# Kernel optimization log

Measured on AMD Instinct MI355X. Metric: run time of the kernel, lower is better.

## Reference

```python
import jax, jax.numpy as jnp
from jax import lax
import numpy as np

G = 18          # grid_dim
NB = 1.0        # num_bins
SIG = 0.6       # sigma
NA = 6          # num_atoms
B = 64          # structures in batch
APB = 512       # atoms per structure
N = B * APB
SIGP2 = 2.0 * (SIG * NB) ** 2  # 2*sigma_p^2


def setup_inputs() -> dict:
    key = jax.random.key(0)
    ks = list(jax.random.split(key, 24))
    # structured atom tensor: sorted batch idx, random atom type, uniform coords
    bidx = jnp.repeat(jnp.arange(B), APB).astype(jnp.float32)
    atype = jax.random.randint(ks[0], (N,), 0, NA).astype(jnp.float32)
    pos = jax.random.uniform(ks[1], (N, 3), minval=-8.5, maxval=8.5)
    x = jnp.concatenate([bidx[:, None], atype[:, None], pos], axis=1)

    def w(k, shape, fan_in):
        return jax.random.normal(k, shape, jnp.float32) * (1.0 / np.sqrt(fan_in))

    d = {"x": x, "batch_size": B}
    chans = [(6, 16), (16, 32), (32, 64)]
    for i, (ci, co) in enumerate(chans):
        d[f"conv_w{i}"] = w(ks[2 + i], (co, ci, 3, 3, 3), ci * 27)
        d[f"conv_b{i}"] = jnp.zeros((co,), jnp.float32)
        d[f"bn_g{i}"] = jnp.ones((co,), jnp.float32)
        d[f"bn_b{i}"] = jnp.zeros((co,), jnp.float32)
    d["mlp_w0"] = w(ks[10], (512, 512), 512); d["mlp_b0"] = jnp.zeros((512,), jnp.float32)
    d["bn1_g"] = jnp.ones((512,), jnp.float32); d["bn1_b"] = jnp.zeros((512,), jnp.float32)
    d["mlp_w1"] = w(ks[11], (256, 512), 512); d["mlp_b1"] = jnp.zeros((256,), jnp.float32)
    d["bn2_g"] = jnp.ones((256,), jnp.float32); d["bn2_b"] = jnp.zeros((256,), jnp.float32)
    d["mlp_w2"] = w(ks[12], (100, 256), 256); d["mlp_b2"] = jnp.zeros((100,), jnp.float32)
    d["head_w"] = w(ks[13], (20, 100), 100); d["head_b"] = jnp.zeros((20,), jnp.float32)
    return d


def _leaky(v):
    return jnp.where(v >= 0, v, 0.01 * v)  # LeakyReLU(0.01)


def _bn(v, g, b, axes):
    # train-mode batchnorm: batch stats, biased var, eps=1e-5; channel axis = 1
    m = v.mean(axes, keepdims=True)
    var = v.var(axes, keepdims=True)
    sh = [1] * v.ndim
    sh[1] = -1
    return (v - m) / jnp.sqrt(var + 1e-5) * g.reshape(sh) + b.reshape(sh)


def _blur(x, batch_size):
    # gaussian_blurring: per-atom normalized gaussian splat onto [B, NA, G, G, G]
    grid = jnp.linspace(-G / 2 * NB + NB / 2, G / 2 * NB - NB / 2, G)
    xx, yy, zz = jnp.meshgrid(grid, grid, grid, indexing='ij')
    coords = jnp.stack([xx.ravel(), yy.ravel(), zz.ravel()], axis=1)  # [V,3]
    pos = x[:, 2:5]                                                   # [N,3]
    # squared distances [N,V] via expansion (avoids [N,V,3] intermediate)
    d2 = ((pos ** 2).sum(1, keepdims=True)
          + (coords ** 2).sum(1)[None, :]
          - 2.0 * pos @ coords.T)
    dens = jnp.exp(-d2 / SIGP2)                         # [N,V]
    dens = dens / (dens.sum(1, keepdims=True) + 1e-6)   # normalize per atom over voxels
    seg = x[:, 0].astype(jnp.int32) * NA + x[:, 1].astype(jnp.int32)
    fields = jax.ops.segment_sum(dens, seg, num_segments=batch_size * NA)
    return fields.reshape(batch_size, NA, G, G, G)


def _forward(x, batch_size, conv_w0, conv_b0, bn_g0, bn_b0, conv_w1, conv_b1, bn_g1, bn_b1,
             conv_w2, conv_b2, bn_g2, bn_b2, mlp_w0, mlp_b0, bn1_g, bn1_b,
             mlp_w1, mlp_b1, bn2_g, bn2_b, mlp_w2, mlp_b2, head_w, head_b):
    h = _blur(x, batch_size)  # [B,6,18,18,18]
    for cw, cb, g, b in ((conv_w0, conv_b0, bn_g0, bn_b0),
                         (conv_w1, conv_b1, bn_g1, bn_b1),
                         (conv_w2, conv_b2, bn_g2, bn_b2)):
        h = lax.conv_general_dilated(h, cw, (1, 1, 1), 'SAME',
                                     dimension_numbers=('NCDHW', 'OIDHW', 'NCDHW'))
        h = h + cb[None, :, None, None, None]
        h = lax.reduce_window(h, -jnp.inf, lax.max, (1, 1, 2, 2, 2), (1, 1, 2, 2, 2), 'VALID')
        h = _leaky(_bn(h, g, b, (0, 2, 3, 4)))
    h = h.reshape(h.shape[0], -1)                                   # [B,512]
    h = _leaky(_bn(h @ mlp_w0.T + mlp_b0, bn1_g, bn1_b, (0,)))
    h = _leaky(_bn(h @ mlp_w1.T + mlp_b1, bn2_g, bn2_b, (0,)))
    h = h @ mlp_w2.T + mlp_b2                                       # [B,100]
    return _leaky(h) @ head_w.T + head_b                            # header -> [B,20]


def reference(x, batch_size, conv_w0, conv_b0, bn_g0, bn_b0, conv_w1, conv_b1, bn_g1, bn_b1,
              conv_w2, conv_b2, bn_g2, bn_b2, mlp_w0, mlp_b0, bn1_g, bn1_b,
              mlp_w1, mlp_b1, bn2_g, bn2_b, mlp_w2, mlp_b2, head_w, head_b):
    return _forward(x, batch_size, conv_w0, conv_b0, bn_g0, bn_b0, conv_w1, conv_b1,
                    bn_g1, bn_b1, conv_w2, conv_b2, bn_g2, bn_b2, mlp_w0, mlp_b0,
                    bn1_g, bn1_b, mlp_w1, mlp_b1, bn2_g, bn2_b, mlp_w2, mlp_b2,
                    head_w, head_b)
```

## Files before the change

### kernel.cpp

```cpp
#include <hip/hip_runtime.h>
#include <math.h>

#define BATCH 64
#define APB 512
#define NA 6
#define NG 5832

__device__ __forceinline__ float leaky(float v){ return v >= 0.f ? v : 0.01f*v; }

__global__ __launch_bounds__(64) void atom_sort(const float* __restrict__ x,
                                                int* __restrict__ dst,
                                                int* __restrict__ seg_start,
                                                int* __restrict__ seg_count)
{
  int batch = blockIdx.x;
  int lane  = threadIdx.x;
  int tyc[8];
  int cnt[NA];
  #pragma unroll
  for (int t = 0; t < NA; t++) cnt[t] = 0;
  #pragma unroll
  for (int c = 0; c < 8; c++){
    int a = batch*APB + c*64 + lane;
    int ty = (int)x[(size_t)a*5 + 1];
    tyc[c] = ty;
    #pragma unroll
    for (int t = 0; t < NA; t++){
      unsigned long long m = __ballot(ty == t);
      cnt[t] += __popcll(m);
    }
  }
  int pre[NA+1];
  pre[0] = 0;
  #pragma unroll
  for (int t = 0; t < NA; t++) pre[t+1] = pre[t] + cnt[t];
  if (lane < NA){
    seg_start[batch*NA + lane] = batch*APB + pre[lane];
    seg_count[batch*NA + lane] = cnt[lane];
  }
  int run[NA];
  #pragma unroll
  for (int t = 0; t < NA; t++) run[t] = pre[t];
  unsigned long long below = (lane == 0) ? 0ull : ((~0ull) >> (64 - lane));
  #pragma unroll
  for (int c = 0; c < 8; c++){
    int a = batch*APB + c*64 + lane;
    int ty = tyc[c];
    int rank = 0;
    #pragma unroll
    for (int t = 0; t < NA; t++){
      unsigned long long m = __ballot(ty == t);
      if (ty == t) rank = run[t] + __popcll(m & below);
      run[t] += __popcll(m);
    }
    dst[a] = batch*APB + rank;
  }
}

__global__ __launch_bounds__(256) void blur_prep(const float* __restrict__ x,
                                                 const int* __restrict__ dst,
                                                 float* __restrict__ tab)
{
  int a = blockIdx.x*256 + threadIdx.x;
  if (a >= BATCH*APB) return;
  const float* row = x + (size_t)a*5;
  float p0 = row[2], p1 = row[3], p2 = row[4];
  float e[54];
  float s0 = 0.f, s1 = 0.f, s2 = 0.f;
  #pragma unroll
  for (int i = 0; i < 18; i++){
    float g = (float)i - 8.5f;
    float d0 = p0 - g, d1 = p1 - g, d2 = p2 - g;
    float v0 = __expf(d0*d0 * (-1.f/0.72f));
    float v1 = __expf(d1*d1 * (-1.f/0.72f));
    float v2 = __expf(d2*d2 * (-1.f/0.72f));
    e[i] = v0; e[18+i] = v1; e[36+i] = v2;
    s0 += v0; s1 += v1; s2 += v2;
  }
  float inv = 1.f / (s0*s1*s2 + 1e-6f);
  float* tp = tab + (size_t)dst[a]*64;
  #pragma unroll
  for (int i = 0; i < 18; i++) tp[i] = e[i]*inv;
  tp[18] = 0.f; tp[19] = 0.f;
  #pragma unroll
  for (int i = 0; i < 18; i++) tp[20+i] = e[18+i];
  #pragma unroll
  for (int i = 0; i < 18; i++) tp[40+i] = e[36+i];
}

__global__ __launch_bounds__(192) void blur_accum(const float* __restrict__ tab,
                                                  const int* __restrict__ seg_start,
                                                  const int* __restrict__ seg_count,
                                                  float* __restrict__ fields)
{
  int bid  = blockIdx.x;
  int seg  = bid >> 1;
  int half = bid & 1;
  int tid = threadIdx.x;
  bool act = tid < 162;
  int ix = half*9 + tid/18;
  int iy = tid % 18;

  float acc[18];
  #pragma unroll
  for (int k = 0; k < 18; k++) acc[k] = 0.f;

  int start = seg_start[seg], count = seg_count[seg];
  const float* tb = tab + (size_t)start*64;

  int j = 0;
  for (; j + 3 < count; j += 4){
    const float* t0 = tb + (size_t)(j+0)*64;
    const float* t1 = tb + (size_t)(j+1)*64;
    const float* t2 = tb + (size_t)(j+2)*64;
    const float* t3 = tb + (size_t)(j+3)*64;
    float e0 = t0[ix]*t0[20+iy];
    float e1 = t1[ix]*t1[20+iy];
    float e2 = t2[ix]*t2[20+iy];
    float e3 = t3[ix]*t3[20+iy];
    #pragma unroll
    for (int k = 0; k < 18; k++){
      float a = acc[k];
      a = fmaf(e0, t0[40+k], a);
      a = fmaf(e1, t1[40+k], a);
      a = fmaf(e2, t2[40+k], a);
      a = fmaf(e3, t3[40+k], a);
      acc[k] = a;
    }
  }
  for (; j < count; j++){
    const float* t0 = tb + (size_t)j*64;
    float e0 = t0[ix]*t0[20+iy];
    #pragma unroll
    for (int k = 0; k < 18; k++)
      acc[k] = fmaf(e0, t0[40+k], acc[k]);
  }
  if (act){
    float* fo = fields + (size_t)seg*NG + (size_t)(ix*18 + iy)*18;
    #pragma unroll
    for (int k = 0; k < 18; k++) fo[k] = acc[k];
  }
}

__global__ __launch_bounds__(256) void transpose_fields(const float* __restrict__ fields,
                                                        float* __restrict__ ft)
{
  __shared__ float tile[64*162];
  int bid = blockIdx.x;
  int t = bid / 36; int r = bid - t*36;
  int gz = r >> 1, gyh = r & 1;
  int tid = threadIdx.x;

  for (int idx = tid; idx < 64*162; idx += 256){
    int b = idx / 162; int c = idx - b*162;
    tile[idx] = fields[(size_t)(b*NA + t)*NG + gz*324 + gyh*162 + c];
  }
  __syncthreads();
  for (int idx = tid; idx < 9*5*64; idx += 256){
    int r2 = idx >> 6; int b = idx & 63;
    int gy = r2 / 5, xq = r2 - gy*5;
    int x0 = xq*4;
    const float* tp = &tile[b*162 + gy*18];
    float4 v;
    v.x = (x0   < 18) ? tp[x0]   : 0.f;
    v.y = (x0+1 < 18) ? tp[x0+1] : 0.f;
    v.z = (x0+2 < 18) ? tp[x0+2] : 0.f;
    v.w = (x0+3 < 18) ? tp[x0+3] : 0.f;
    *(float4*)(ft + ((((size_t)t*18 + gz)*18 + (gyh*9+gy))*5 + xq)*256 + b*4) = v;
  }
}

__global__ __launch_bounds__(64) void conv0t_kernel(const float* __restrict__ ft,
                                                    const float* __restrict__ w,
                                                    const float* __restrict__ bias,
                                                    float* __restrict__ out,
                                                    float* __restrict__ part)
{
  int bid = blockIdx.x;
  int l = (bid & 7)*324 + (bid >> 3);
  int oc = l & 15, xh = (l >> 4) & 1;
  int sp = l >> 5;
  int pz = sp / 9, py = sp - pz*9;
  int lane = threadIdx.x;

  float acc[2][2][10];
  #pragma unroll
  for (int i=0;i<2;i++)
    #pragma unroll
    for (int j=0;j<2;j++)
      #pragma unroll
      for (int k=0;k<10;k++) acc[i][j][k]=0.f;

  float bb = bias[oc];
  float s = 0.f, s2 = 0.f;
  float* op = out + (((size_t)oc*9 + pz)*9 + py)*3*256 + lane*4;

  if (xh == 0){
    #pragma unroll
    for (int ic = 0; ic < 6; ic++){
      float wr[27];
      #pragma unroll
      for (int k = 0; k < 27; k++) wr[k] = w[(oc*6+ic)*27 + k];
      #pragma unroll
      for (int zl = 0; zl < 4; zl++){
        int gz = 2*pz - 1 + zl;
        bool vz = ((unsigned)gz < 18u);
        int gzc = vz ? gz : (gz < 0 ? 0 : 17);
        #pragma unroll
        for (int yl = 0; yl < 4; yl++){
          int gy = 2*py - 1 + yl;
          bool v = vz && ((unsigned)gy < 18u);
          int gyc = ((unsigned)gy < 18u) ? gy : (gy < 0 ? 0 : 17);
          const float* rp = ft + (((size_t)ic*18 + gzc)*18 + gyc)*5*256 + lane*4;
          float4 A0 = *(const float4*)(rp);
          float4 A1 = *(const float4*)(rp + 256);
          float4 A2 = *(const float4*)(rp + 512);
          float xv[13];
          xv[0] = 0.f;
          *(float4*)&xv[1] = A0; *(float4*)&xv[5] = A1; *(float4*)&xv[9] = A2;
          #pragma unroll
          for (int czl = 0; czl < 2; czl++){
            const int dz = zl - czl; if (dz < 0 || dz > 2) continue;
            #pragma unroll
            for (int cyl = 0; cyl < 2; cyl++){
              const int dy = yl - cyl; if (dy < 0 || dy > 2) continue;
              const int wb = dz*9 + dy*3;
              const float w0 = v ? wr[wb]   : 0.f;
              const float w1 = v ? wr[wb+1] : 0.f;
              const float w2 = v ? wr[wb+2] : 0.f;
              #pragma unroll
              for (int cx = 0; cx < 10; cx++){
                float a = acc[czl][cyl][cx];
                a = fmaf(xv[cx],   w0, a);
                a = fmaf(xv[cx+1], w1, a);
                a = fmaf(xv[cx+2], w2, a);
                acc[czl][cyl][cx] = a;
              }
            }
          }
        }
      }
    }
    float px[5];
    #pragma unroll
    for (int p = 0; p < 5; p++){
      float m = fmaxf(fmaxf(acc[0][0][2*p], acc[0][0][2*p+1]),
                      fmaxf(acc[0][1][2*p], acc[0][1][2*p+1]));
      m = fmaxf(m, fmaxf(fmaxf(acc[1][0][2*p], acc[1][0][2*p+1]),
                         fmaxf(acc[1][1][2*p], acc[1][1][2*p+1])));
      px[p] = m + bb;
      s += px[p]; s2 += px[p]*px[p];
    }
    *(float4*)(op) = make_float4(px[0], px[1], px[2], px[3]);
    op[256] = px[4];
  } else {
    #pragma unroll
    for (int ic = 0; ic < 6; ic++){
      float wr[27];
      #pragma unroll
      for (int k = 0; k < 27; k++) wr[k] = w[(oc*6+ic)*27 + k];
      #pragma unroll
      for (int zl = 0; zl < 4; zl++){
        int gz = 2*pz - 1 + zl;
        bool vz = ((unsigned)gz < 18u);
        int gzc = vz ? gz : (gz < 0 ? 0 : 17);
        #pragma unroll
        for (int yl = 0; yl < 4; yl++){
          int gy = 2*py - 1 + yl;
          bool v = vz && ((unsigned)gy < 18u);
          int gyc = ((unsigned)gy < 18u) ? gy : (gy < 0 ? 0 : 17);
          const float* rp = ft + (((size_t)ic*18 + gzc)*18 + gyc)*5*256 + lane*4;
          float4 A2 = *(const float4*)(rp + 512);
          float4 A3 = *(const float4*)(rp + 768);
          float4 A4 = *(const float4*)(rp + 1024);
          float win[12];
          *(float4*)&win[0] = A2; *(float4*)&win[4] = A3; *(float4*)&win[8] = A4;
          #pragma unroll
          for (int czl = 0; czl < 2; czl++){
            const int dz = zl - czl; if (dz < 0 || dz > 2) continue;
            #pragma unroll
            for (int cyl = 0; cyl < 2; cyl++){
              const int dy = yl - cyl; if (dy < 0 || dy > 2) continue;
              const int wb = dz*9 + dy*3;
              const float w0 = v ? wr[wb]   : 0.f;
              const float w1 = v ? wr[wb+1] : 0.f;
              const float w2 = v ? wr[wb+2] : 0.f;
              #pragma unroll
              for (int cl = 0; cl < 8; cl++){
                float a = acc[czl][cyl][cl];
                a = fmaf(win[cl+1], w0, a);
                a = fmaf(win[cl+2], w1, a);
                a = fmaf(win[cl+3], w2, a);
                acc[czl][cyl][cl] = a;
              }
            }
          }
        }
      }
    }
    float px[4];
    #pragma unroll
    for (int p = 0; p < 4; p++){
      float m = fmaxf(fmaxf(acc[0][0][2*p], acc[0][0][2*p+1]),
                      fmaxf(acc[0][1][2*p], acc[0][1][2*p+1]));
      m = fmaxf(m, fmaxf(fmaxf(acc[1][0][2*p], acc[1][0][2*p+1]),
                         fmaxf(acc[1][1][2*p], acc[1][1][2*p+1])));
      px[p] = m + bb;
      s += px[p]; s2 += px[p]*px[p];
    }
    op[256+1] = px[0]; op[256+2] = px[1]; op[256+3] = px[2]; op[512] = px[3];
  }
  #pragma unroll
  for (int d = 32; d > 0; d >>= 1){ s += __shfl_down(s, d); s2 += __shfl_down(s2, d); }
  if (lane == 0){
    int pi = oc*162 + sp*2 + xh;
    part[(size_t)pi*2] = s; part[(size_t)pi*2+1] = s2;
  }
}

__global__ __launch_bounds__(256) void conv1t_kernel(const float* __restrict__ p0t,
                                                     const float* __restrict__ w,
                                                     const float* __restrict__ bias,
                                                     const float* __restrict__ sc,
                                                     const float* __restrict__ sh,
                                                     float* __restrict__ out,
                                                     float* __restrict__ part)
{
  __shared__ float red[3*32*64];
  int bid = blockIdx.x;
  int l = (bid & 7)*64 + (bid >> 3);
  int oc = l & 31;
  int sp = l >> 5;
  int pz = sp >> 2, py = sp & 3;
  int tid = threadIdx.x;
  int wid = tid >> 6, lane = tid & 63;

  float acc[2][2][8];
  #pragma unroll
  for (int i=0;i<2;i++)
    #pragma unroll
    for (int j=0;j<2;j++)
      #pragma unroll
      for (int k=0;k<8;k++) acc[i][j][k]=0.f;

  const float* wbp = w + (size_t)oc*16*27;
  #pragma unroll
  for (int icl = 0; icl < 4; icl++){
    int ic = wid*4 + icl;
    float wr[27];
    #pragma unroll
    for (int k = 0; k < 27; k++) wr[k] = wbp[ic*27 + k];
    float s0v = sc[ic], h0v = sh[ic];
    #pragma unroll
    for (int zl = 0; zl < 4; zl++){
      int gz = 2*pz - 1 + zl;
      bool vz = ((unsigned)gz < 9u);
      int gzc = vz ? gz : 0;
      #pragma unroll
      for (int yl = 0; yl < 4; yl++){
        int gy = 2*py - 1 + yl;
        bool v = vz && ((unsigned)gy < 9u);
        int gyc = ((unsigned)gy < 9u) ? gy : 0;
        const float* rp = p0t + (((size_t)ic*9 + gzc)*9 + gyc)*3*256 + lane*4;
        float4 A0 = *(const float4*)(rp);
        float4 A1 = *(const float4*)(rp + 256);
        float  A2 = rp[512];
        float xv[10];
        xv[0]=0.f;
        xv[1]=leaky(fmaf(A0.x, s0v, h0v)); xv[2]=leaky(fmaf(A0.y, s0v, h0v));
        xv[3]=leaky(fmaf(A0.z, s0v, h0v)); xv[4]=leaky(fmaf(A0.w, s0v, h0v));
        xv[5]=leaky(fmaf(A1.x, s0v, h0v)); xv[6]=leaky(fmaf(A1.y, s0v, h0v));
        xv[7]=leaky(fmaf(A1.z, s0v, h0v)); xv[8]=leaky(fmaf(A1.w, s0v, h0v));
        xv[9]=leaky(fmaf(A2,   s0v, h0v));
        #pragma unroll
        for (int czl = 0; czl < 2; czl++){
          const int dz = zl - czl; if (dz < 0 || dz > 2) continue;
          #pragma unroll
          for (int cyl = 0; cyl < 2; cyl++){
            const int dy = yl - cyl; if (dy < 0 || dy > 2) continue;
            const int wb = dz*9 + dy*3;
            const float w0 = v ? wr[wb]   : 0.f;
            const float w1 = v ? wr[wb+1] : 0.f;
            const float w2 = v ? wr[wb+2] : 0.f;
            #pragma unroll
            for (int cx = 0; cx < 8; cx++){
              float a = acc[czl][cyl][cx];
              a = fmaf(xv[cx],   w0, a);
              a = fmaf(xv[cx+1], w1, a);
              a = fmaf(xv[cx+2], w2, a);
              acc[czl][cyl][cx] = a;
            }
          }
        }
      }
    }
  }
  if (wid > 0){
    #pragma unroll
    for (int i=0;i<2;i++)
      #pragma unroll
      for (int j=0;j<2;j++)
        #pragma unroll
        for (int k=0;k<8;k++)
          red[(((wid-1)*32) + (i*2+j)*8 + k)*64 + lane] = acc[i][j][k];
  }
  __syncthreads();
  if (wid == 0){
    #pragma unroll
    for (int q = 0; q < 3; q++)
      #pragma unroll
      for (int i=0;i<2;i++)
        #pragma unroll
        for (int j=0;j<2;j++)
          #pragma unroll
          for (int k=0;k<8;k++)
            acc[i][j][k] += red[((q*32) + (i*2+j)*8 + k)*64 + lane];

    float bb = bias[oc];
    float px[4];
    float s = 0.f, s2 = 0.f;
    #pragma unroll
    for (int p = 0; p < 4; p++){
      float m = fmaxf(fmaxf(acc[0][0][2*p], acc[0][0][2*p+1]),
                      fmaxf(acc[0][1][2*p], acc[0][1][2*p+1]));
      m = fmaxf(m, fmaxf(fmaxf(acc[1][0][2*p], acc[1][0][2*p+1]),
                         fmaxf(acc[1][1][2*p], acc[1][1][2*p+1])));
      px[p] = m + bb;
      s += px[p]; s2 += px[p]*px[p];
    }
    *(float4*)(out + (((size_t)oc*4 + pz)*4 + py)*256 + lane*4) =
        make_float4(px[0], px[1], px[2], px[3]);
    #pragma unroll
    for (int d = 32; d > 0; d >>= 1){ s += __shfl_down(s, d); s2 += __shfl_down(s2, d); }
    if (lane == 0){
      int pi = oc*16 + sp;
      part[(size_t)pi*2] = s; part[(size_t)pi*2+1] = s2;
    }
  }
}

__global__ __launch_bounds__(512) void conv2t_kernel(const float* __restrict__ p1t,
                                                     const float* __restrict__ w,
                                                     const float* __restrict__ bias,
                                                     const float* __restrict__ sc,
                                                     const float* __restrict__ sh,
                                                     float* __restrict__ out)
{
  __shared__ float red[6*8*64];
  int bid = blockIdx.x;
  int l = (bid & 7)*32 + (bid >> 3);
  int oc = l & 63;
  int q  = l >> 6;
  int Pz = q >> 1, Py = q & 1;
  int tid = threadIdx.x;
  int wid = tid >> 6, lane = tid & 63;
  int Px = wid >> 2, icq = wid & 3;

  float acc[2][2][2];
  #pragma unroll
  for (int i=0;i<2;i++)
    #pragma unroll
    for (int j=0;j<2;j++)
      #pragma unroll
      for (int k=0;k<2;k++) acc[i][j][k]=0.f;

  const float* wbp = w + (size_t)oc*32*27;
  #pragma unroll
  for (int icl = 0; icl < 8; icl++){
    int ic = icq*8 + icl;
    float wr[27];
    #pragma unroll
    for (int k = 0; k < 27; k++) wr[k] = wbp[ic*27 + k];
    float s1v = sc[ic], h1v = sh[ic];
    #pragma unroll
    for (int zl = 0; zl < 4; zl++){
      int gz = 2*Pz - 1 + zl;
      bool vz = ((unsigned)gz < 4u);
      int gzc = vz ? gz : (gz < 0 ? 0 : 3);
      #pragma unroll
      for (int yl = 0; yl < 4; yl++){
        int gy = 2*Py - 1 + yl;
        bool v = vz && ((unsigned)gy < 4u);
        int gyc = ((unsigned)gy < 4u) ? gy : (gy < 0 ? 0 : 3);
        float4 f = *(const float4*)(p1t + (((size_t)ic*4 + gzc)*4 + gyc)*256 + lane*4);
        float b0 = leaky(fmaf(f.x, s1v, h1v));
        float b1 = leaky(fmaf(f.y, s1v, h1v));
        float b2 = leaky(fmaf(f.z, s1v, h1v));
        float b3 = leaky(fmaf(f.w, s1v, h1v));
        float win[4];
        if (Px == 0){ win[0]=0.f; win[1]=b0; win[2]=b1; win[3]=b2; }
        else        { win[0]=b1;  win[1]=b2; win[2]=b3; win[3]=0.f; }
        #pragma unroll
        for (int czl = 0; czl < 2; czl++){
          const int dz = zl - czl; if (dz < 0 || dz > 2) continue;
          #pragma unroll
          for (int cyl = 0; cyl < 2; cyl++){
            const int dy = yl - cyl; if (dy < 0 || dy > 2) continue;
            const int wb = dz*9 + dy*3;
            const float w0 = v ? wr[wb]   : 0.f;
            const float w1 = v ? wr[wb+1] : 0.f;
            const float w2 = v ? wr[wb+2] : 0.f;
            #pragma unroll
            for (int cxl = 0; cxl < 2; cxl++){
              float a = acc[czl][cyl][cxl];
              a = fmaf(win[cxl],   w0, a);
              a = fmaf(win[cxl+1], w1, a);
              a = fmaf(win[cxl+2], w2, a);
              acc[czl][cyl][cxl] = a;
            }
          }
        }
      }
    }
  }
  if (icq > 0){
    #pragma unroll
    for (int i=0;i<2;i++)
      #pragma unroll
      for (int j=0;j<2;j++)
        #pragma unroll
        for (int k=0;k<2;k++)
          red[(((Px*3 + icq-1)*8) + (i*2+j)*2 + k)*64 + lane] = acc[i][j][k];
  }
  __syncthreads();
  if (icq == 0){
    #pragma unroll
    for (int qq = 0; qq < 3; qq++)
      #pragma unroll
      for (int i=0;i<2;i++)
        #pragma unroll
        for (int j=0;j<2;j++)
          #pragma unroll
          for (int k=0;k<2;k++)
            acc[i][j][k] += red[(((Px*3 + qq)*8) + (i*2+j)*2 + k)*64 + lane];

    float bb = bias[oc];
    float m = fmaxf(fmaxf(acc[0][0][0], acc[0][0][1]), fmaxf(acc[0][1][0], acc[0][1][1]));
    m = fmaxf(m, fmaxf(fmaxf(acc[1][0][0], acc[1][0][1]), fmaxf(acc[1][1][0], acc[1][1][1])));
    out[((size_t)oc*8 + Pz*4 + Py*2 + Px)*64 + lane] = m + bb;
  }
}

template<int C, int N>
__global__ __launch_bounds__(256) void stats_final(const float* __restrict__ part,
                                                   float* __restrict__ scale,
                                                   float* __restrict__ shift,
                                                   const float* __restrict__ g,
                                                   const float* __restrict__ bb,
                                                   float n)
{
  int c = blockIdx.x;
  float s = 0.f, s2 = 0.f;
  for (int i = threadIdx.x; i < N; i += 256){
    s  += part[(size_t)(c*N + i)*2];
    s2 += part[(size_t)(c*N + i)*2 + 1];
  }
  #pragma unroll
  for (int d = 32; d > 0; d >>= 1){ s += __shfl_down(s, d); s2 += __shfl_down(s2, d); }
  __shared__ float rs[4], rq[4];
  int lane = threadIdx.x & 63, wid = threadIdx.x >> 6;
  if (lane == 0){ rs[wid] = s; rq[wid] = s2; }
  __syncthreads();
  if (threadIdx.x == 0){
    float ts = rs[0]+rs[1]+rs[2]+rs[3];
    float tq = rq[0]+rq[1]+rq[2]+rq[3];
    float m = ts / n;
    float var = tq / n - m*m;
    float is = rsqrtf(var + 1e-5f);
    float scv = is * g[c];
    scale[c] = scv;
    shift[c] = bb[c] - m * scv;
  }
}

__global__ __launch_bounds__(256) void bn2t_kernel(const float* __restrict__ p2t,
                                                   const float* __restrict__ g,
                                                   const float* __restrict__ bb,
                                                   float* __restrict__ scale,
                                                   float* __restrict__ shift)
{
  int gt = blockIdx.x*256 + threadIdx.x;
  int c = gt >> 6, lane = gt & 63;
  if (c >= 64) return;
  const float* p = p2t + (size_t)c*512;
  float s = 0.f, s2 = 0.f;
  #pragma unroll
  for (int i = 0; i < 8; i++){ float v = p[i*64 + lane]; s += v; s2 += v*v; }
  #pragma unroll
  for (int d = 32; d > 0; d >>= 1){ s += __shfl_down(s, d); s2 += __shfl_down(s2, d); }
  if (lane == 0){
    float m = s * (1.f/512.f);
    float var = s2 * (1.f/512.f) - m*m;
    float scv = rsqrtf(var + 1e-5f) * g[c];
    scale[c] = scv;
    shift[c] = bb[c] - m*scv;
  }
}

__global__ __launch_bounds__(256) void fc0bn_kernel(const float* __restrict__ p2t,
                                                    const float* __restrict__ W,
                                                    const float* __restrict__ bias,
                                                    const float* __restrict__ sc,
                                                    const float* __restrict__ sh,
                                                    const float* __restrict__ g,
                                                    const float* __restrict__ bb,
                                                    float* __restrict__ y0t)
{
  __shared__ float red[3][64];
  int f = blockIdx.x;
  int wid = threadIdx.x >> 6, r = threadIdx.x & 63;
  const float* wr = W + (size_t)f*512;
  float a = 0.f;
  for (int c = wid*16; c < wid*16 + 16; c++){
    float s = sc[c], h = sh[c];
    #pragma unroll
    for (int jj = 0; jj < 8; jj++){
      int i = c*8 + jj;
      float xv = leaky(fmaf(p2t[(size_t)i*64 + r], s, h));
      a = fmaf(xv, wr[i], a);
    }
  }
  if (wid > 0) red[wid-1][r] = a;
  __syncthreads();
  if (wid == 0){
    a += red[0][r] + red[1][r] + red[2][r] + bias[f];
    float s1 = a, s2 = a*a;
    #pragma unroll
    for (int d = 32; d > 0; d >>= 1){ s1 += __shfl_down(s1, d); s2 += __shfl_down(s2, d); }
    s1 = __shfl(s1, 0); s2 = __shfl(s2, 0);
    float m = s1 * (1.f/64.f);
    float var = s2 * (1.f/64.f) - m*m;
    float is = rsqrtf(var + 1e-5f);
    y0t[(size_t)f*64 + r] = leaky((a - m) * is * g[f] + bb[f]);
  }
}

__global__ __launch_bounds__(512) void fc1bn_kernel(const float* __restrict__ y0t,
                                                    const float* __restrict__ W,
                                                    const float* __restrict__ bias,
                                                    const float* __restrict__ g,
                                                    const float* __restrict__ bb,
                                                    float* __restrict__ y1t)
{
  __shared__ float red[7][64];
  int f = blockIdx.x;
  int wid = threadIdx.x >> 6, r = threadIdx.x & 63;
  const float* wr = W + (size_t)f*512;
  float a = 0.f;
  #pragma unroll 8
  for (int i = wid*64; i < wid*64 + 64; i++)
    a = fmaf(y0t[(size_t)i*64 + r], wr[i], a);
  if (wid > 0) red[wid-1][r] = a;
  __syncthreads();
  if (wid == 0){
    #pragma unroll
    for (int q = 0; q < 7; q++) a += red[q][r];
    a += bias[f];
    float s1 = a, s2 = a*a;
    #pragma unroll
    for (int d = 32; d > 0; d >>= 1){ s1 += __shfl_down(s1, d); s2 += __shfl_down(s2, d); }
    s1 = __shfl(s1, 0); s2 = __shfl(s2, 0);
    float m = s1 * (1.f/64.f);
    float var = s2 * (1.f/64.f) - m*m;
    float is = rsqrtf(var + 1e-5f);
    y1t[(size_t)f*64 + r] = leaky((a - m) * is * g[f] + bb[f]);
  }
}

__global__ __launch_bounds__(256) void fc2_kernel(const float* __restrict__ y1t,
                                                  const float* __restrict__ W,
                                                  const float* __restrict__ bias,
                                                  float* __restrict__ y2t)
{
  __shared__ float red[3][64];
  int f = blockIdx.x;
  int wid = threadIdx.x >> 6, r = threadIdx.x & 63;
  const float* wr = W + (size_t)f*256;
  float a = 0.f;
  #pragma unroll 8
  for (int i = wid*64; i < wid*64 + 64; i++)
    a = fmaf(y1t[(size_t)i*64 + r], wr[i], a);
  if (wid > 0) red[wid-1][r] = a;
  __syncthreads();
  if (wid == 0){
    a += red[0][r] + red[1][r] + red[2][r];
    y2t[(size_t)f*64 + r] = leaky(a + bias[f]);
  }
}

__global__ __launch_bounds__(256) void head_kernel(const float* __restrict__ y2t,
                                                   const float* __restrict__ W,
                                                   const float* __restrict__ bias,
                                                   float* __restrict__ out)
{
  int gt = blockIdx.x*256 + threadIdx.x;
  int oo = gt >> 6, r = gt & 63;
  if (oo >= 20) return;
  const float* wr = W + (size_t)oo*100;
  float a = 0.f;
  #pragma unroll 4
  for (int i = 0; i < 100; i++)
    a = fmaf(y2t[(size_t)i*64 + r], wr[i], a);
  out[(size_t)r*20 + oo] = a + bias[oo];
}

extern "C" void kernel_launch(void* const* d_in, const int* in_sizes, int n_in,
                              void* d_out, int out_size, void* d_ws, size_t ws_size,
                              hipStream_t stream)
{
  const float* x   = (const float*)d_in[0];
  const float* cw0 = (const float*)d_in[2];  const float* cb0 = (const float*)d_in[3];
  const float* g0  = (const float*)d_in[4];  const float* bb0 = (const float*)d_in[5];
  const float* cw1 = (const float*)d_in[6];  const float* cb1 = (const float*)d_in[7];
  const float* g1  = (const float*)d_in[8];  const float* bb1 = (const float*)d_in[9];
  const float* cw2 = (const float*)d_in[10]; const float* cb2 = (const float*)d_in[11];
  const float* g2  = (const float*)d_in[12]; const float* bb2 = (const float*)d_in[13];
  const float* mw0 = (const float*)d_in[14]; const float* mb0 = (const float*)d_in[15];
  const float* g3  = (const float*)d_in[16]; const float* bb3 = (const float*)d_in[17];
  const float* mw1 = (const float*)d_in[18]; const float* mb1 = (const float*)d_in[19];
  const float* g4  = (const float*)d_in[20]; const float* bb4 = (const float*)d_in[21];
  const float* mw2 = (const float*)d_in[22]; const float* mb2 = (const float*)d_in[23];
  const float* hw  = (const float*)d_in[24]; const float* hb  = (const float*)d_in[25];

  float* ws     = (float*)d_ws;
  float* tab    = ws;
  float* ft     = ws;
  int*   dst    = (int*)(ws + 2097152);
  int*   sstart = dst + 32768;
  int*   scount = sstart + 384;
  float* fields = ws + 2488320;
  float* p0t    = fields;
  float* rest   = fields + 2239488;
  float* p1t    = rest;
  float* p2t    = p1t + 131072;
  float* y0t    = p2t + 32768;
  float* y1t    = y0t + 32768;
  float* y2t    = y1t + 16384;
  float* part   = y2t + 6400;
  float* sc0    = part + 6144;
  float* sh0    = sc0 + 16;
  float* sc1    = sh0 + 16;
  float* sh1    = sc1 + 32;
  float* sc2    = sh1 + 32;
  float* sh2    = sc2 + 64;
  float* outp   = (float*)d_out;

  atom_sort<<<64, 64, 0, stream>>>(x, dst, sstart, scount);
  blur_prep<<<128, 256, 0, stream>>>(x, dst, tab);
  blur_accum<<<768, 192, 0, stream>>>(tab, sstart, scount, fields);
  transpose_fields<<<216, 256, 0, stream>>>(fields, ft);

  conv0t_kernel<<<2592, 64, 0, stream>>>(ft, cw0, cb0, p0t, part);
  stats_final<16,162><<<16, 256, 0, stream>>>(part, sc0, sh0, g0, bb0, 64.f*729.f);

  conv1t_kernel<<<512, 256, 0, stream>>>(p0t, cw1, cb1, sc0, sh0, p1t, part);
  stats_final<32,16><<<32, 256, 0, stream>>>(part, sc1, sh1, g1, bb1, 64.f*64.f);

  conv2t_kernel<<<256, 512, 0, stream>>>(p1t, cw2, cb2, sc1, sh1, p2t);
  bn2t_kernel<<<16, 256, 0, stream>>>(p2t, g2, bb2, sc2, sh2);

  fc0bn_kernel<<<512, 256, 0, stream>>>(p2t, mw0, mb0, sc2, sh2, g3, bb3, y0t);
  fc1bn_kernel<<<256, 512, 0, stream>>>(y0t, mw1, mb1, g4, bb4, y1t);
  fc2_kernel<<<100, 256, 0, stream>>>(y1t, mw2, mb2, y2t);
  head_kernel<<<5, 256, 0, stream>>>(y2t, hw, hb, outp);
}
```

Measured before the change: 164.7 us.

## Fuse field transpose into blur accumulation by writing transposed layout directly

The blur accumulation kernel now stores its per-voxel sums straight into the batch-interleaved, x-padded layout that the first convolution reads, using float4 stores. This removes the separate transpose kernel and the round trip of the full density grid through global memory. Workspace offsets are rearranged so the conv outputs and the transposed fields no longer overlap. The direct stores are strided per lane (16-byte writes spread far apart), so write coalescing is worse than in the old contiguous stores.

```diff
diff --git a/kernel.cpp b/kernel.cpp
--- a/kernel.cpp
+++ b/kernel.cpp
@@ -91,11 +91,12 @@
 __global__ __launch_bounds__(192) void blur_accum(const float* __restrict__ tab,
                                                   const int* __restrict__ seg_start,
                                                   const int* __restrict__ seg_count,
-                                                  float* __restrict__ fields)
+                                                  float* __restrict__ ft)
 {
   int bid  = blockIdx.x;
   int seg  = bid >> 1;
   int half = bid & 1;
+  int batch = seg / NA, t = seg - batch*NA;
   int tid = threadIdx.x;
   bool act = tid < 162;
   int ix = half*9 + tid/18;
@@ -136,37 +137,12 @@
       acc[k] = fmaf(e0, t0[40+k], acc[k]);
   }
   if (act){
-    float* fo = fields + (size_t)seg*NG + (size_t)(ix*18 + iy)*18;
-    #pragma unroll
-    for (int k = 0; k < 18; k++) fo[k] = acc[k];
-  }
-}
-
-__global__ __launch_bounds__(256) void transpose_fields(const float* __restrict__ fields,
-                                                        float* __restrict__ ft)
-{
-  __shared__ float tile[64*162];
-  int bid = blockIdx.x;
-  int t = bid / 36; int r = bid - t*36;
-  int gz = r >> 1, gyh = r & 1;
-  int tid = threadIdx.x;
-
-  for (int idx = tid; idx < 64*162; idx += 256){
-    int b = idx / 162; int c = idx - b*162;
-    tile[idx] = fields[(size_t)(b*NA + t)*NG + gz*324 + gyh*162 + c];
-  }
-  __syncthreads();
-  for (int idx = tid; idx < 9*5*64; idx += 256){
-    int r2 = idx >> 6; int b = idx & 63;
-    int gy = r2 / 5, xq = r2 - gy*5;
-    int x0 = xq*4;
-    const float* tp = &tile[b*162 + gy*18];
-    float4 v;
-    v.x = (x0   < 18) ? tp[x0]   : 0.f;
-    v.y = (x0+1 < 18) ? tp[x0+1] : 0.f;
-    v.z = (x0+2 < 18) ? tp[x0+2] : 0.f;
-    v.w = (x0+3 < 18) ? tp[x0+3] : 0.f;
-    *(float4*)(ft + ((((size_t)t*18 + gz)*18 + (gyh*9+gy))*5 + xq)*256 + b*4) = v;
+    float* fo = ft + ((((size_t)t*18 + ix)*18 + iy)*5)*256 + (size_t)batch*4;
+    *(float4*)(fo)        = make_float4(acc[0],  acc[1],  acc[2],  acc[3]);
+    *(float4*)(fo + 256)  = make_float4(acc[4],  acc[5],  acc[6],  acc[7]);
+    *(float4*)(fo + 512)  = make_float4(acc[8],  acc[9],  acc[10], acc[11]);
+    *(float4*)(fo + 768)  = make_float4(acc[12], acc[13], acc[14], acc[15]);
+    *(float4*)(fo + 1024) = make_float4(acc[16], acc[17], 0.f, 0.f);
   }
 }
 
@@ -724,14 +700,11 @@
 
   float* ws     = (float*)d_ws;
   float* tab    = ws;
-  float* ft     = ws;
   int*   dst    = (int*)(ws + 2097152);
   int*   sstart = dst + 32768;
   int*   scount = sstart + 384;
-  float* fields = ws + 2488320;
-  float* p0t    = fields;
-  float* rest   = fields + 2239488;
-  float* p1t    = rest;
+  float* p0t    = ws;
+  float* p1t    = ws + 995328;
   float* p2t    = p1t + 131072;
   float* y0t    = p2t + 32768;
   float* y1t    = y0t + 32768;
@@ -743,12 +716,12 @@
   float* sh1    = sc1 + 32;
   float* sc2    = sh1 + 32;
   float* sh2    = sc2 + 64;
+  float* ft     = ws + 2488320;
   float* outp   = (float*)d_out;
 
   atom_sort<<<64, 64, 0, stream>>>(x, dst, sstart, scount);
   blur_prep<<<128, 256, 0, stream>>>(x, dst, tab);
-  blur_accum<<<768, 192, 0, stream>>>(tab, sstart, scount, fields);
-  transpose_fields<<<216, 256, 0, stream>>>(fields, ft);
+  blur_accum<<<768, 192, 0, stream>>>(tab, sstart, scount, ft);
 
   conv0t_kernel<<<2592, 64, 0, stream>>>(ft, cw0, cb0, p0t, part);
   stats_final<16,162><<<16, 256, 0, stream>>>(part, sc0, sh0, g0, bb0, 64.f*729.f);
```

Measured after the change: 154.4 us, median of 2. 1.07x faster.
